# Performance work log

Hardware: AMD Instinct MI355X
Metric: run time of the kernel (lower is better)

## Reference

```python
import jax, jax.numpy as jnp
import numpy as np

KERNEL_SIZE = 5
SIGMA = 1.0
DARK_KS = 15


def _gaussian_kernel():
    x = jnp.arange(KERNEL_SIZE, dtype=jnp.float32) - KERNEL_SIZE // 2
    phi = jnp.exp(-0.5 * x * x / (SIGMA ** 2))
    phi = phi / (phi.sum() + 0.001)
    k2d = jnp.outer(phi, phi)                       # [5,5]
    return jnp.tile(k2d[None, None], (3, 1, 1, 1))  # [3,1,5,5] OIHW depthwise


def _tanh01(v):
    return jnp.tanh(v) * 0.5 + 0.5


def setup_inputs() -> dict:
    key = jax.random.key(0)
    k1, k2, k3 = jax.random.split(key, 3)
    # keep x strictly positive so x**param has well-defined gradients
    x = jax.random.uniform(k1, (16, 3, 512, 512), dtype=jnp.float32, minval=0.01, maxval=1.0)
    output1 = jax.random.normal(k2, (16, 7), dtype=jnp.float32)
    output2 = jax.random.normal(k3, (16, 4), dtype=jnp.float32)
    return {"x": x, "output1": output1, "output2": output2}


def reference(x, output1, output2):
    N, C, H, W = x.shape

    # ---- parameter squashing (clip_range + softmax weights) ----
    o1 = jnp.concatenate([
        _tanh01(output1[:, 0:1]) * 0.25 + 1.0,   # gamma param in [1, 1.25]
        _tanh01(output1[:, 1:2]) * 0.9 + 0.1,    # contrast alpha (dead branch)
        _tanh01(output1[:, 2:3]) * 2.0,          # sharpen lamda in [0, 2]
        _tanh01(output1[:, 3:4]),                # dehaze w in [0, 1]
        _tanh01(output1[:, 4:7]) * 0.1 + 0.95,   # WB gains in [0.95, 1.05]
    ], axis=1)
    o2 = jax.nn.softmax(_tanh01(output2), axis=1)  # [N,4] branch weights

    param = o1[:, 0][:, None, None, None]
    lamda = o1[:, 2][:, None, None, None]
    w = o1[:, 3][:, None, None, None]
    wb_params = o1[:, 4:7][:, :, None, None]

    # ---- WB ----
    x1 = jnp.clip(x * wb_params, 0.0, 1.0)

    # ---- GAMMA ----
    x2 = jnp.clip(x ** param + 0.001, 0.0, 1.0)

    # ---- SHARPEN (depthwise 5x5 gaussian blur, unsharp mask) ----
    gk = _gaussian_kernel()
    blur = jax.lax.conv_general_dilated(
        x, gk, window_strides=(1, 1), padding=((2, 2), (2, 2)),
        feature_group_count=3,
        dimension_numbers=("NCHW", "OIHW", "NCHW"))
    blur = jnp.clip(blur, 0.0, 1.0)
    x4 = jnp.clip(x + lamda * (x - blur), 0.0, 1.0)

    # ---- DEHAZE ----
    minc = jnp.min(x, axis=1, keepdims=True)  # [N,1,H,W]
    # avg_pool2d k=15 s=1 p=7 with count_include_pad=True -> sum window / 225
    dark = jax.lax.reduce_window(
        minc, 0.0, jax.lax.add, (1, 1, DARK_KS, DARK_KS), (1, 1, 1, 1),
        padding=[(0, 0), (0, 0), (DARK_KS // 2, DARK_KS // 2), (DARK_KS // 2, DARK_KS // 2)]
    ) / float(DARK_KS * DARK_KS)
    top_k = int(H * W * 0.05)
    flat_dark = dark.reshape(N, -1)
    _, top_idx = jax.lax.top_k(flat_dark, top_k)            # [N, top_k]
    flat_img = x.reshape(N, C, -1)
    sel = jnp.take_along_axis(flat_img, top_idx[:, None, :], axis=2)  # [N,C,top_k]
    A = sel.mean(axis=2)[:, :, None, None]                  # atmospheric light
    trans = 1.0 - w * dark
    trans = jnp.where(trans > 0.1, trans, jnp.float32(0.1))
    x5 = jnp.clip((x - A) / (trans + 0.001) + A, 0.0, 1.0)

    # ---- weighted combination (contrast branch is computed but unused upstream) ----
    w0 = o2[:, 0][:, None, None, None]
    w1 = o2[:, 1][:, None, None, None]
    w2 = o2[:, 2][:, None, None, None]
    w3 = o2[:, 3][:, None, None, None]
    x_sum = x + 0.1 * (w0 * x1 + w1 * x2 + w2 * x4 + w3 * x5)
    x_sum = x_sum / (jnp.sum(o2, axis=1)[:, None, None, None] + 0.001)

    # ---- per-sample per-channel min-max normalization ----
    min_vals = jnp.min(x_sum, axis=(2, 3), keepdims=True)
    max_vals = jnp.max(x_sum, axis=(2, 3), keepdims=True)
    return (x_sum - min_vals) / (max_vals - min_vals + 1e-07)
```

## Files before the change

### kernel.cpp

```cpp
#include <hip/hip_runtime.h>
#include <math.h>

#define NS   16
#define HH   512
#define WW   512
#define HW   (HH*WW)
#define TOPK 13107
#define NBIN 4096

#define O_O1   0
#define O_O2   112
#define O_DEN  176
#define O_KN   304
#define O_A    320
#define O_MMP  512
#define O_DARK 33280


#define G0 0.054466787f
#define G1 0.244103071f
#define G2 0.402457854f

__device__ __forceinline__ float tanh01(float v) { return tanhf(v)*0.5f + 0.5f; }
__device__ __forceinline__ float clamp01(float v) { return fminf(fmaxf(v, 0.0f), 1.0f); }
__device__ __forceinline__ int dark_bin(float v) {
  int b = (int)(v * (float)NBIN);
  return b > (NBIN-1) ? (NBIN-1) : (b < 0 ? 0 : b);
}

__global__ void k_zero(unsigned* __restrict__ hist) {
  int i = blockIdx.x * 256 + threadIdx.x;
  uint4 z; z.x = 0u; z.y = 0u; z.z = 0u; z.w = 0u;
  ((uint4*)hist)[i] = z;
}

__global__ void __launch_bounds__(256)
k_dark(const float* __restrict__ x, float* __restrict__ wsf, unsigned* __restrict__ hist) {
  __shared__ __align__(16) float sm[4096 + 46*64];
  float* minc = sm;
  unsigned* lh = (unsigned*)sm;
  float* hsum = sm + 4096;
  int tid = threadIdx.x;
  int w0 = blockIdx.x * 64, h0 = blockIdx.y * 32, n = blockIdx.z;
  const float* xb = x + (size_t)n*3*HW;

  for (int i = tid; i < 46*20; i += 256) {
    int r = i / 20, q = i - r*20;
    int hm = h0 - 7 + r, wc = w0 - 8 + 4*q;
    float4 v; v.x = 0.f; v.y = 0.f; v.z = 0.f; v.w = 0.f;
    if (hm >= 0 && hm < HH && wc >= 0 && wc < WW) {
      size_t o = (size_t)hm*WW + wc;
      float4 a = *(const float4*)&xb[o];
      float4 b = *(const float4*)&xb[HW + o];
      float4 c = *(const float4*)&xb[2*HW + o];
      v.x = fminf(fminf(a.x,b.x),c.x); v.y = fminf(fminf(a.y,b.y),c.y);
      v.z = fminf(fminf(a.z,b.z),c.z); v.w = fminf(fminf(a.w,b.w),c.w);
    }
    *(float4*)&minc[r*80 + 4*q] = v;
  }
  __syncthreads();
  for (int i = tid; i < 46*16; i += 256) {
    int r = i >> 4, c4 = (i & 15) * 4;
    const float4* mr = (const float4*)&minc[r*80];
    int qb = c4 >> 2;
    float m[20];
    #pragma unroll
    for (int t = 0; t < 5; ++t) {
      float4 v = mr[qb + t];
      m[4*t] = v.x; m[4*t+1] = v.y; m[4*t+2] = v.z; m[4*t+3] = v.w;
    }
    float s = 0.f;
    #pragma unroll
    for (int j = 1; j <= 15; ++j) s += m[j];
    float4 o;
    o.x = s; s += m[16] - m[1];
    o.y = s; s += m[17] - m[2];
    o.z = s; s += m[18] - m[3];
    o.w = s;
    *(float4*)&hsum[r*64 + c4] = o;
  }
  __syncthreads();
  for (int i = tid; i < NBIN; i += 256) lh[i] = 0u;
  __syncthreads();
  {
    int c = tid & 63, ty = tid >> 6, r0 = ty * 8;
    float s = 0.f;
    #pragma unroll
    for (int j = 0; j < 15; ++j) s += hsum[(r0 + j)*64 + c];
    float* dk = wsf + O_DARK + (size_t)n*HW;
    #pragma unroll
    for (int i = 0; i < 8; ++i) {
      int r = r0 + i;
      float v = s * (1.0f/225.0f);
      dk[(size_t)(h0 + r)*WW + w0 + c] = v;
      atomicAdd(&lh[dark_bin(v)], 1u);
      if (i < 7) s += hsum[(r + 15)*64 + c] - hsum[r*64 + c];
    }
  }
  __syncthreads();
  unsigned* gh = hist + n*NBIN;
  for (int i = tid; i < NBIN; i += 256) { unsigned v = lh[i]; if (v) atomicAdd(&gh[i], v); }
}

__global__ void __launch_bounds__(256)
k_asum(const float* __restrict__ x, const float* __restrict__ wsf,
       const unsigned* __restrict__ hist, unsigned* __restrict__ wsu,
       float* __restrict__ part) {
  __shared__ __align__(16) unsigned lh[NBIN];
  __shared__ unsigned spp[256];
  __shared__ int sh_bsel; __shared__ unsigned sh_kn;
  __shared__ float bl[4][7];
  int tid = threadIdx.x;
  int n = blockIdx.x >> 6, chunk = blockIdx.x & 63;
  const uint4* gh4 = (const uint4*)(hist + n*NBIN);
  unsigned ps = 0;
  #pragma unroll
  for (int k = 0; k < 4; ++k) {
    uint4 v = gh4[tid*4 + k];
    *(uint4*)&lh[tid*16 + 4*k] = v;
    ps += v.x + v.y + v.z + v.w;
  }
  spp[tid] = ps;
  __syncthreads();
  if (tid == 0) {
    const unsigned K = TOPK;
    unsigned cum = 0; int bsel = 0;
    for (int t = 255; t >= 0; --t) {
      if (cum + spp[t] >= K) {
        bsel = t*16;
        for (int b = t*16 + 15; b >= t*16; --b) {
          if (cum + lh[b] >= K) { bsel = b; break; }
          cum += lh[b];
        }
        break;
      }
      cum += spp[t];
    }
    sh_bsel = bsel; sh_kn = K - cum;
    if (chunk == 0) wsu[O_KN + n] = K - cum;
  }
  __syncthreads();
  int bsel = sh_bsel;
  const float4* db = (const float4*)(wsf + O_DARK + (size_t)n*HW + (size_t)chunk*4096);
  const float4* x0 = (const float4*)(x + (size_t)n*3*HW + (size_t)chunk*4096);
  const float4* x1 = x0 + HW/4;
  const float4* x2 = x0 + HW/2;
  float s0=0,s1=0,s2=0,e0=0,e1=0,e2=0,ec=0;
  #pragma unroll
  for (int k = 0; k < 4; ++k) {
    int idx = k*256 + tid;
    float4 d = db[idx], a = x0[idx], b = x1[idx], c = x2[idx];
    #define ACC(DX, AX, BX, CX) { \
      int bb = dark_bin(DX); \
      bool gt = (bb > bsel), eq = (bb == bsel); \
      s0 += gt ? AX : 0.f; s1 += gt ? BX : 0.f; s2 += gt ? CX : 0.f; \
      e0 += eq ? AX : 0.f; e1 += eq ? BX : 0.f; e2 += eq ? CX : 0.f; \
      ec += eq ? 1.f : 0.f; }
    ACC(d.x, a.x, b.x, c.x) ACC(d.y, a.y, b.y, c.y)
    ACC(d.z, a.z, b.z, c.z) ACC(d.w, a.w, b.w, c.w)
    #undef ACC
  }
  #pragma unroll
  for (int off = 32; off; off >>= 1) {
    s0 += __shfl_down(s0, off); s1 += __shfl_down(s1, off); s2 += __shfl_down(s2, off);
    e0 += __shfl_down(e0, off); e1 += __shfl_down(e1, off); e2 += __shfl_down(e2, off);
    ec += __shfl_down(ec, off);
  }
  int wave = tid >> 6, lane = tid & 63;
  if (lane == 0) {
    bl[wave][0]=s0; bl[wave][1]=s1; bl[wave][2]=s2;
    bl[wave][3]=e0; bl[wave][4]=e1; bl[wave][5]=e2; bl[wave][6]=ec;
  }
  __syncthreads();
  if (tid < 7) {
    float v = bl[0][tid] + bl[1][tid] + bl[2][tid] + bl[3][tid];
    part[blockIdx.x*8 + tid] = v;
  }
}

__global__ void k_areduce(const float* __restrict__ part, const unsigned* __restrict__ wsu,
                          float* __restrict__ wsf, const float* __restrict__ o1,
                          const float* __restrict__ o2) {
  int n = blockIdx.x, t = threadIdx.x;
  const float* p = part + (size_t)(n*64 + t)*8;
  float s0=p[0], s1=p[1], s2=p[2], e0=p[3], e1=p[4], e2=p[5], ec=p[6];
  #pragma unroll
  for (int off = 32; off; off >>= 1) {
    s0 += __shfl_down(s0, off); s1 += __shfl_down(s1, off); s2 += __shfl_down(s2, off);
    e0 += __shfl_down(e0, off); e1 += __shfl_down(e1, off); e2 += __shfl_down(e2, off);
    ec += __shfl_down(ec, off);
  }
  if (t == 0) {
    float kn = (float)wsu[O_KN + n];
    float ce = fmaxf(ec, 1.0f);
    wsf[O_A + n*3 + 0] = (s0 + kn * (e0 / ce)) * (1.0f/(float)TOPK);
    wsf[O_A + n*3 + 1] = (s1 + kn * (e1 / ce)) * (1.0f/(float)TOPK);
    wsf[O_A + n*3 + 2] = (s2 + kn * (e2 / ce)) * (1.0f/(float)TOPK);
    wsf[O_O1+n*7+0] = tanh01(o1[n*7+0])*0.25f + 1.0f;
    wsf[O_O1+n*7+1] = tanh01(o1[n*7+1])*0.9f  + 0.1f;
    wsf[O_O1+n*7+2] = tanh01(o1[n*7+2])*2.0f;
    wsf[O_O1+n*7+3] = tanh01(o1[n*7+3]);
    wsf[O_O1+n*7+4] = tanh01(o1[n*7+4])*0.1f + 0.95f;
    wsf[O_O1+n*7+5] = tanh01(o1[n*7+5])*0.1f + 0.95f;
    wsf[O_O1+n*7+6] = tanh01(o1[n*7+6])*0.1f + 0.95f;
    float q0 = expf(tanh01(o2[n*4+0]));
    float q1 = expf(tanh01(o2[n*4+1]));
    float q2 = expf(tanh01(o2[n*4+2]));
    float q3 = expf(tanh01(o2[n*4+3]));
    float s = q0+q1+q2+q3;
    q0 /= s; q1 /= s; q2 /= s; q3 /= s;
    wsf[O_O2+n*4+0]=q0; wsf[O_O2+n*4+1]=q1; wsf[O_O2+n*4+2]=q2; wsf[O_O2+n*4+3]=q3;
    wsf[O_DEN+n] = (q0+q1+q2+q3) + 0.001f;
  }
}

__global__ void __launch_bounds__(256)
k_main(const float* __restrict__ x, float* __restrict__ wsf, float* __restrict__ out) {
  __shared__ __align__(16) float xs[20*72];
  __shared__ __align__(16) float hb[20*64];
  __shared__ float rmn[4], rmx[4];
  int tid = threadIdx.x;
  int w0 = blockIdx.x * 64, h0 = blockIdx.y * 16;
  int z = blockIdx.z, n = z / 3, c = z % 3;
  const float* xc = x + (size_t)z*HW;
  for (int i = tid; i < 360; i += 256) {
    int r = i / 18, q = i - r*18;
    int gh = h0 - 2 + r, gw = w0 - 4 + 4*q;
    float4 v; v.x = 0.f; v.y = 0.f; v.z = 0.f; v.w = 0.f;
    if (gh >= 0 && gh < HH && gw >= 0 && gw < WW)
      v = *(const float4*)&xc[(size_t)gh*WW + gw];
    *(float4*)&xs[r*72 + 4*q] = v;
  }
  __syncthreads();
  for (int i = tid; i < 320; i += 256) {
    int r = i >> 4, c4 = (i & 15) * 4;
    const float4* xr = (const float4*)&xs[r*72];
    int qb = c4 >> 2;
    float4 A4 = xr[qb], B4 = xr[qb+1], C4 = xr[qb+2];
    float m2=A4.z, m3=A4.w, m4=B4.x, m5=B4.y, m6=B4.z, m7=B4.w, m8=C4.x, m9=C4.y;
    float4 o;
    o.x = G0*(m2+m6) + G1*(m3+m5) + G2*m4;
    o.y = G0*(m3+m7) + G1*(m4+m6) + G2*m5;
    o.z = G0*(m4+m8) + G1*(m5+m7) + G2*m6;
    o.w = G0*(m5+m9) + G1*(m6+m8) + G2*m7;
    *(float4*)&hb[r*64 + c4] = o;
  }
  __syncthreads();
  float param = wsf[O_O1 + n*7 + 0];
  float lamda = wsf[O_O1 + n*7 + 2];
  float wpar  = wsf[O_O1 + n*7 + 3];
  float wb    = wsf[O_O1 + n*7 + 4 + c];
  float q0 = wsf[O_O2 + n*4 + 0], q1 = wsf[O_O2 + n*4 + 1];
  float q2 = wsf[O_O2 + n*4 + 2], q3 = wsf[O_O2 + n*4 + 3];
  float rden = 1.0f / wsf[O_DEN + n];
  float A   = wsf[O_A + n*3 + c];
  int r = tid >> 4, c4 = (tid & 15) * 4;
  float4 xv = *(const float4*)&xs[(r+2)*72 + c4 + 4];
  float4 b0 = *(const float4*)&hb[(r+0)*64 + c4];
  float4 b1 = *(const float4*)&hb[(r+1)*64 + c4];
  float4 b2 = *(const float4*)&hb[(r+2)*64 + c4];
  float4 b3 = *(const float4*)&hb[(r+3)*64 + c4];
  float4 b4 = *(const float4*)&hb[(r+4)*64 + c4];
  const float* dark = wsf + O_DARK + (size_t)n*HW;
  float4 dk = *(const float4*)&dark[(size_t)(h0+r)*WW + w0 + c4];
  float4 osum;
  float mnv = 3.4e38f, mxv = -3.4e38f;
  #define PIX(OX, XV, B0, B1, B2, B3, B4, DK) { \
    float blur = clamp01(G0*(B0+B4) + G1*(B1+B3) + G2*B2); \
    float x4v = clamp01(XV + lamda*(XV - blur)); \
    float x1v = clamp01(XV * wb); \
    float x2v = clamp01(__expf(param*__logf(XV)) + 0.001f); \
    float tr = 1.0f - wpar*DK; tr = tr > 0.1f ? tr : 0.1f; \
    float x5v = clamp01((XV - A)/(tr + 0.001f) + A); \
    OX = (XV + 0.1f*(q0*x1v + q1*x2v + q2*x4v + q3*x5v)) * rden; \
    mnv = fminf(mnv, OX); mxv = fmaxf(mxv, OX); }
  PIX(osum.x, xv.x, b0.x, b1.x, b2.x, b3.x, b4.x, dk.x)
  PIX(osum.y, xv.y, b0.y, b1.y, b2.y, b3.y, b4.y, dk.y)
  PIX(osum.z, xv.z, b0.z, b1.z, b2.z, b3.z, b4.z, dk.z)
  PIX(osum.w, xv.w, b0.w, b1.w, b2.w, b3.w, b4.w, dk.w)
  #undef PIX
  *(float4*)&out[(size_t)z*HW + (size_t)(h0+r)*WW + w0 + c4] = osum;
  #pragma unroll
  for (int off = 32; off; off >>= 1) {
    mnv = fminf(mnv, __shfl_down(mnv, off));
    mxv = fmaxf(mxv, __shfl_down(mxv, off));
  }
  int wave = tid >> 6, lane = tid & 63;
  if (lane == 0) { rmn[wave] = mnv; rmx[wave] = mxv; }
  __syncthreads();
  if (tid == 0) {
    mnv = fminf(fminf(rmn[0], rmn[1]), fminf(rmn[2], rmn[3]));
    mxv = fmaxf(fmaxf(rmx[0], rmx[1]), fmaxf(rmx[2], rmx[3]));
    int bxy = blockIdx.y * 8 + blockIdx.x;
    wsf[O_MMP + z*512 + bxy]       = mnv;
    wsf[O_MMP + z*512 + 256 + bxy] = mxv;
  }
}

__global__ void __launch_bounds__(256)
k_norm(float* __restrict__ out, const float* __restrict__ wsf) {
  __shared__ float rmn[4], rmx[4];
  int tid = threadIdx.x;
  int nc = blockIdx.x >> 8;
  float mn = wsf[O_MMP + nc*512 + tid];
  float mx = wsf[O_MMP + nc*512 + 256 + tid];
  #pragma unroll
  for (int off = 32; off; off >>= 1) {
    mn = fminf(mn, __shfl_down(mn, off));
    mx = fmaxf(mx, __shfl_down(mx, off));
  }
  int wave = tid >> 6, lane = tid & 63;
  if (lane == 0) { rmn[wave] = mn; rmx[wave] = mx; }
  __syncthreads();
  mn = fminf(fminf(rmn[0], rmn[1]), fminf(rmn[2], rmn[3]));
  mx = fmaxf(fmaxf(rmx[0], rmx[1]), fmaxf(rmx[2], rmx[3]));
  float sc = 1.0f / (mx - mn + 1e-7f);
  int i4 = blockIdx.x * 256 + tid;
  float4 v = ((const float4*)out)[i4];
  v.x = (v.x - mn) * sc; v.y = (v.y - mn) * sc;
  v.z = (v.z - mn) * sc; v.w = (v.w - mn) * sc;
  ((float4*)out)[i4] = v;
}

extern "C" void kernel_launch(void* const* d_in, const int* in_sizes, int n_in,
                              void* d_out, int out_size, void* d_ws, size_t ws_size,
                              hipStream_t stream) {
  const float* x  = (const float*)d_in[0];
  const float* o1 = (const float*)d_in[1];
  const float* o2 = (const float*)d_in[2];
  float* out = (float*)d_out;
  float* wsf = (float*)d_ws;
  unsigned* wsu = (unsigned*)d_ws;
  unsigned* hist = (unsigned*)(out + (size_t)16*HW);
  float* part = out + (size_t)17*HW;

  k_zero<<<dim3(64), dim3(256), 0, stream>>>(hist);
  k_dark<<<dim3(8, 16, 16), dim3(256), 0, stream>>>(x, wsf, hist);
  k_asum<<<dim3(1024), dim3(256), 0, stream>>>(x, wsf, hist, wsu, part);
  k_areduce<<<dim3(16), dim3(64), 0, stream>>>(part, wsu, wsf, o1, o2);
  k_main<<<dim3(8, 32, 48), dim3(256), 0, stream>>>(x, wsf, out);
  k_norm<<<dim3(12288), dim3(256), 0, stream>>>(out, wsf);
}
```

Baseline: 192.1 us.

## Hoist top-k bin selection and min-max reduce into tiny kernels, aggregate histogram atomics

Splits the per-sample threshold-bin search out of k_asum into a separate 16-block kernel, so the 1024 asum blocks no longer each reload a 4096-bin histogram and scan it serially. The min/max partial reduction likewise moves out of the 12288 k_norm blocks into a 48-block kernel, and k_norm now processes 8 float4s per thread with fewer blocks. Shared-memory histogram atomics in k_dark are aggregated per wavefront via ballot/match loops to reduce contention. The cost is two extra kernel launches and a possibly longer ballot loop when bins are diverse.

```diff
diff --git a/kernel.cpp b/kernel.cpp
--- a/kernel.cpp
+++ b/kernel.cpp
@@ -11,8 +11,11 @@
 #define O_O1   0
 #define O_O2   112
 #define O_DEN  176
+#define O_BSEL 288
 #define O_KN   304
 #define O_A    320
+#define O_MIN  368
+#define O_MAX  416
 #define O_MMP  512
 #define O_DARK 33280
 
@@ -84,6 +87,7 @@
   __syncthreads();
   {
     int c = tid & 63, ty = tid >> 6, r0 = ty * 8;
+    int lane = tid & 63;
     float s = 0.f;
     #pragma unroll
     for (int j = 0; j < 15; ++j) s += hsum[(r0 + j)*64 + c];
@@ -93,7 +97,17 @@
       int r = r0 + i;
       float v = s * (1.0f/225.0f);
       dk[(size_t)(h0 + r)*WW + w0 + c] = v;
-      atomicAdd(&lh[dark_bin(v)], 1u);
+      int b = dark_bin(v);
+      bool need = true;
+      while (__any(need)) {
+        unsigned long long mn = __ballot(need);
+        int src = __ffsll(mn) - 1;
+        int bsel = __shfl(b, src);
+        bool same = need && (b == bsel);
+        unsigned long long mm = __ballot(same);
+        if (lane == src) atomicAdd(&lh[bsel], (unsigned)__popcll(mm));
+        if (same) need = false;
+      }
       if (i < 7) s += hsum[(r + 15)*64 + c] - hsum[r*64 + c];
     }
   }
@@ -102,17 +116,12 @@
   for (int i = tid; i < NBIN; i += 256) { unsigned v = lh[i]; if (v) atomicAdd(&gh[i], v); }
 }
 
-__global__ void __launch_bounds__(256)
-k_asum(const float* __restrict__ x, const float* __restrict__ wsf,
-       const unsigned* __restrict__ hist, unsigned* __restrict__ wsu,
-       float* __restrict__ part) {
+__global__ void k_select(const unsigned* __restrict__ hist, unsigned* __restrict__ wsu) {
+  int n = blockIdx.x, tid = threadIdx.x;
+  const unsigned* gh = hist + n*NBIN;
   __shared__ __align__(16) unsigned lh[NBIN];
   __shared__ unsigned spp[256];
-  __shared__ int sh_bsel; __shared__ unsigned sh_kn;
-  __shared__ float bl[4][7];
-  int tid = threadIdx.x;
-  int n = blockIdx.x >> 6, chunk = blockIdx.x & 63;
-  const uint4* gh4 = (const uint4*)(hist + n*NBIN);
+  const uint4* gh4 = (const uint4*)gh;
   unsigned ps = 0;
   #pragma unroll
   for (int k = 0; k < 4; ++k) {
@@ -136,11 +145,18 @@
       }
       cum += spp[t];
     }
-    sh_bsel = bsel; sh_kn = K - cum;
-    if (chunk == 0) wsu[O_KN + n] = K - cum;
-  }
-  __syncthreads();
-  int bsel = sh_bsel;
+    wsu[O_BSEL + n] = (unsigned)bsel;
+    wsu[O_KN + n]   = K - cum;
+  }
+}
+
+__global__ void __launch_bounds__(256)
+k_asum(const float* __restrict__ x, const float* __restrict__ wsf,
+       const unsigned* __restrict__ wsu, float* __restrict__ part) {
+  __shared__ float bl[4][7];
+  int tid = threadIdx.x;
+  int n = blockIdx.x >> 6, chunk = blockIdx.x & 63;
+  int bsel = (int)wsu[O_BSEL + n];
   const float4* db = (const float4*)(wsf + O_DARK + (size_t)n*HW + (size_t)chunk*4096);
   const float4* x0 = (const float4*)(x + (size_t)n*3*HW + (size_t)chunk*4096);
   const float4* x1 = x0 + HW/4;
@@ -172,10 +188,7 @@
     bl[wave][3]=e0; bl[wave][4]=e1; bl[wave][5]=e2; bl[wave][6]=ec;
   }
   __syncthreads();
-  if (tid < 7) {
-    float v = bl[0][tid] + bl[1][tid] + bl[2][tid] + bl[3][tid];
-    part[blockIdx.x*8 + tid] = v;
-  }
+  if (tid < 7) part[blockIdx.x*8 + tid] = bl[0][tid] + bl[1][tid] + bl[2][tid] + bl[3][tid];
 }
 
 __global__ void k_areduce(const float* __restrict__ part, const unsigned* __restrict__ wsu,
@@ -297,13 +310,11 @@
   }
 }
 
-__global__ void __launch_bounds__(256)
-k_norm(float* __restrict__ out, const float* __restrict__ wsf) {
+__global__ void k_mmred(float* __restrict__ wsf) {
+  int z = blockIdx.x, tid = threadIdx.x;
   __shared__ float rmn[4], rmx[4];
-  int tid = threadIdx.x;
-  int nc = blockIdx.x >> 8;
-  float mn = wsf[O_MMP + nc*512 + tid];
-  float mx = wsf[O_MMP + nc*512 + 256 + tid];
+  float mn = wsf[O_MMP + z*512 + tid];
+  float mx = wsf[O_MMP + z*512 + 256 + tid];
   #pragma unroll
   for (int off = 32; off; off >>= 1) {
     mn = fminf(mn, __shfl_down(mn, off));
@@ -312,14 +323,28 @@
   int wave = tid >> 6, lane = tid & 63;
   if (lane == 0) { rmn[wave] = mn; rmx[wave] = mx; }
   __syncthreads();
-  mn = fminf(fminf(rmn[0], rmn[1]), fminf(rmn[2], rmn[3]));
-  mx = fmaxf(fmaxf(rmx[0], rmx[1]), fmaxf(rmx[2], rmx[3]));
+  if (tid == 0) {
+    wsf[O_MIN + z] = fminf(fminf(rmn[0], rmn[1]), fminf(rmn[2], rmn[3]));
+    wsf[O_MAX + z] = fmaxf(fmaxf(rmx[0], rmx[1]), fmaxf(rmx[2], rmx[3]));
+  }
+}
+
+__global__ void __launch_bounds__(256)
+k_norm(float* __restrict__ out, const float* __restrict__ wsf) {
+  int nc = blockIdx.x >> 5;
+  int sub = blockIdx.x & 31;
+  float mn = wsf[O_MIN + nc];
+  float mx = wsf[O_MAX + nc];
   float sc = 1.0f / (mx - mn + 1e-7f);
-  int i4 = blockIdx.x * 256 + tid;
-  float4 v = ((const float4*)out)[i4];
-  v.x = (v.x - mn) * sc; v.y = (v.y - mn) * sc;
-  v.z = (v.z - mn) * sc; v.w = (v.w - mn) * sc;
-  ((float4*)out)[i4] = v;
+  float4* o4 = (float4*)out + (size_t)nc*65536 + (size_t)sub*2048;
+  int tid = threadIdx.x;
+  #pragma unroll
+  for (int k = 0; k < 8; ++k) {
+    float4 v = o4[k*256 + tid];
+    v.x = (v.x - mn) * sc; v.y = (v.y - mn) * sc;
+    v.z = (v.z - mn) * sc; v.w = (v.w - mn) * sc;
+    o4[k*256 + tid] = v;
+  }
 }
 
 extern "C" void kernel_launch(void* const* d_in, const int* in_sizes, int n_in,
@@ -336,8 +361,10 @@
 
   k_zero<<<dim3(64), dim3(256), 0, stream>>>(hist);
   k_dark<<<dim3(8, 16, 16), dim3(256), 0, stream>>>(x, wsf, hist);
-  k_asum<<<dim3(1024), dim3(256), 0, stream>>>(x, wsf, hist, wsu, part);
+  k_select<<<dim3(16), dim3(256), 0, stream>>>(hist, wsu);
+  k_asum<<<dim3(1024), dim3(256), 0, stream>>>(x, wsf, wsu, part);
   k_areduce<<<dim3(16), dim3(64), 0, stream>>>(part, wsu, wsf, o1, o2);
   k_main<<<dim3(8, 32, 48), dim3(256), 0, stream>>>(x, wsf, out);
-  k_norm<<<dim3(12288), dim3(256), 0, stream>>>(out, wsf);
-}
+  k_mmred<<<dim3(48), dim3(256), 0, stream>>>(wsf);
+  k_norm<<<dim3(1536), dim3(256), 0, stream>>>(out, wsf);
+}
```

Measured after the change: 306.5 us. 1.6x slower.
